# Optimization experiments

Hardware: AMD Instinct MI355X
Metric: run time of the kernel (lower is better)

## Reference

```python
import jax, jax.numpy as jnp
import numpy as np

# --- static forest structure: NT complete ternary trees of depth DEPTH ---
BR, DEPTH, NT = 3, 7, 64            # branching factor (=L), edge-levels, num trees
OFF = [(3 ** d - 1) // 2 for d in range(DEPTH + 2)]  # BFS level offsets within a tree
NPT = OFF[DEPTH + 1]                 # nodes per tree = 3280
DIM = NT * NPT                       # total nodes = 209920
C_DIM, NGEN, M_SYM = 8, 8, 128


def build_tree():
    """Returns pos, leaves, batch, roots, levels [(parent_idx, child_idx)], unique-parents per level."""
    base = (np.arange(NT) * NPT)[:, None]
    pos = np.zeros(DIM, dtype=np.int64)
    levels, upar = [], []
    for d in range(1, DEPTH + 1):
        loc = np.arange(OFF[d], OFF[d + 1])
        ch = (base + loc).ravel()                                 # children at depth d (tree-major)
        pa = (base + (OFF[d - 1] + (loc - OFF[d]) // BR)).ravel() # their parents
        pos[ch] = np.tile((loc - OFF[d]) % BR, NT)
        levels.append((pa, ch))
        upar.append((base + np.arange(OFF[d - 1], OFF[d])).ravel())  # unique parents of level d
    leaves = (base + np.arange(OFF[DEPTH], OFF[DEPTH + 1])).ravel()
    batch = np.repeat(np.arange(NT), NPT)
    roots = np.arange(NT) * NPT
    return pos, leaves, batch, roots, levels, upar


def setup_inputs() -> dict:
    key = jax.random.key(0)
    k1, k2, k3, k4, k5 = jax.random.split(key, 5)
    pos_np, leaves_np, batch_np, _, _, _ = build_tree()
    return {
        "lam_A": jax.random.uniform(k1, (C_DIM, C_DIM, BR, NGEN), dtype=jnp.float32),
        "lam_B": jax.random.uniform(k2, (C_DIM, M_SYM, NGEN), dtype=jnp.float32),
        "lam_Pi": jax.random.uniform(k3, (C_DIM, BR, NGEN), dtype=jnp.float32),
        "lam_SP": jax.random.uniform(k4, (BR, NGEN), dtype=jnp.float32),
        "x": jax.random.randint(k5, (DIM,), 0, M_SYM, dtype=jnp.int64),
        "pos": jnp.asarray(pos_np),
        "leaves": jnp.asarray(leaves_np),
        "batch": jnp.asarray(batch_np),
    }


def reference(lam_A, lam_B, lam_Pi, lam_SP, x, pos, leaves, batch):
    # ReversedUpwardDownward (mode='bu') of PosteriorHiddenTreeMarkovModel.
    A = jax.nn.softmax(lam_A, axis=0)   # (C,C,L,G): softmax over first state axis
    Bm = jax.nn.softmax(lam_B, axis=1)  # (C,M,G): softmax over symbols
    Pi = jax.nn.softmax(lam_Pi, axis=0) # (C,L,G)
    SP = jax.nn.softmax(lam_SP, axis=0) # (L,G)
    C, G = A.shape[0], A.shape[-1]
    _, _, _, roots, levels, upar = build_tree()  # static structure

    beta = jnp.zeros((DIM, C, G), lam_A.dtype)
    t_beta = jnp.zeros((DIM, C, G), lam_A.dtype)

    # --- leaves init ---
    Pi_leaves = Pi[:, pos[leaves]]            # (C,Nl,G)
    bl = jnp.transpose(Pi_leaves * Bm[:, x[leaves]], (1, 0, 2))  # (Nl,C,G)
    beta = beta.at[leaves].set(bl / bl.sum(1, keepdims=True))

    # --- upward pass (deepest level first) ---
    for (pa, ch), u in zip(reversed(levels), reversed(upar)):
        SP_ch = SP[pos[ch]][:, None, None, :]                 # (E,1,1,G)
        A_ch = jnp.transpose(A[:, :, pos[ch]], (2, 0, 1, 3))  # (E,C,C,G)
        tb = (SP_ch * A_ch * beta[ch][:, None]).sum(2)        # (E,C,G) sum over child state
        t_beta = t_beta.at[pa].add(tb)
        bu = t_beta[u] * jnp.transpose(Bm[:, x[u]], (1, 0, 2))
        beta = beta.at[u].set(bu / bu.sum(1, keepdims=True))

    # --- downward pass ---
    eps = jnp.zeros((DIM, C, G), lam_A.dtype)
    ell = jnp.zeros((DIM, G), lam_A.dtype)
    eps = eps.at[roots].set(beta[roots])
    for pa, ch in levels:
        SP_ch = SP[pos[ch]]                                   # (E,G)
        A_ch = jnp.transpose(A[:, :, pos[ch]], (2, 0, 1, 3))  # (E,C,C,G)
        trans = SP_ch[:, None, None, :] * A_ch
        ej = (eps[pa][:, :, None, :] * trans * beta[ch][:, None, :, :]
              / t_beta[pa][:, :, None, :])                    # (E,C,C,G) joint posterior
        eps = eps.at[ch].set(ej.sum(1))
        ell = ell.at[ch].add((ej * jnp.log(A_ch)).sum((1, 2))
                             + ej.sum((1, 2)) * jnp.log(SP_ch))
    ell = ell + (eps * jnp.transpose(Bm[:, x], (1, 0, 2))).sum(1)
    ell = ell.at[leaves].add((eps[leaves] * jnp.transpose(jnp.log(Pi_leaves), (1, 0, 2))).sum(1))
    return -jax.ops.segment_sum(ell, batch, num_segments=NT)  # (NT,G)
```

## Files before the change

### kernel.cpp

```cpp
#include <hip/hip_runtime.h>
#include <hip/hip_fp16.h>


namespace {

constexpr int kNPT = 3280;
constexpr int kRS  = 72;
constexpr int kAS  = 68;
constexpr unsigned kMAGIC  = 0x13579BDFu;
constexpr unsigned kMAGIC2 = 0x2468ACEFu;
__device__ __constant__ int LO[6] = {0, 1, 4, 13, 40, 121};
__device__ __constant__ int P3[5] = {1, 3, 9, 27, 81};

#define AGENT_LD(p)    __hip_atomic_load((p), __ATOMIC_RELAXED, __HIP_MEMORY_SCOPE_AGENT)
#define AGENT_ST(p, v) __hip_atomic_store((p), (v), __ATOMIC_RELAXED, __HIP_MEMORY_SCOPE_AGENT)

__device__ __forceinline__ void bm_row(const float* __restrict__ pBmg, int xv,
                                       float* m)
{
    const float4 r0 = *(const float4*)(pBmg + (xv << 3));
    const float4 r1 = *(const float4*)(pBmg + (xv << 3) + 4);
    m[0] = r0.x; m[1] = r0.y; m[2] = r0.z; m[3] = r0.w;
    m[4] = r1.x; m[5] = r1.y; m[6] = r1.z; m[7] = r1.w;
}

__device__ __forceinline__ void leaf_beta(const float* __restrict__ sPi,
                                          const float* __restrict__ pBmg,
                                          int p, int xv, int g, float* b)
{
    float m[8];
    bm_row(pBmg, xv, m);
    float s = 0.f;
    #pragma unroll
    for (int c = 0; c < 8; ++c) {
        b[c] = sPi[(c * 3 + p) * 8 + g] * m[c];
        s += b[c];
    }
    float ig = __builtin_amdgcn_rcpf(s);
    #pragma unroll
    for (int c = 0; c < 8; ++c) b[c] *= ig;
}

__device__ __forceinline__ float norm_mul(const float* __restrict__ pBmg,
                                          int xv, float* acc)
{
    float m[8];
    bm_row(pBmg, xv, m);
    float s = 0.f;
    #pragma unroll
    for (int i = 0; i < 8; ++i) { acc[i] *= m[i]; s += acc[i]; }
    return s;
}

__device__ __forceinline__ void matvec_acc(const float* __restrict__ arow,
                                           const float* __restrict__ bj,
                                           float spg, float* acc)
{
    #pragma unroll
    for (int j = 0; j < 8; ++j) {
        float4 a0 = *(const float4*)(arow + j * 8);
        float4 a1 = *(const float4*)(arow + j * 8 + 4);
        float cjv = spg * bj[j];
        acc[0] = fmaf(a0.x, cjv, acc[0]); acc[1] = fmaf(a0.y, cjv, acc[1]);
        acc[2] = fmaf(a0.z, cjv, acc[2]); acc[3] = fmaf(a0.w, cjv, acc[3]);
        acc[4] = fmaf(a1.x, cjv, acc[4]); acc[5] = fmaf(a1.y, cjv, acc[5]);
        acc[6] = fmaf(a1.z, cjv, acc[6]); acc[7] = fmaf(a1.w, cjv, acc[7]);
    }
}

__global__ __launch_bounds__(256, 2)
void fused(const float* __restrict__ lamA, const float* __restrict__ lamB,
           const float* __restrict__ lamPi, const float* __restrict__ lamSP,
           const int* __restrict__ x, float* __restrict__ out,
           unsigned* __restrict__ sy, float* __restrict__ bmG,
           float* __restrict__ b3, float* __restrict__ e3)
{
    const int tid = threadIdx.x, w = tid >> 6, lane = tid & 63;
    const int n = lane >> 3, g = lane & 7;
    __shared__ __align__(16) float sAg[24 * kAS];
    __shared__ __align__(16) float sLAg[24 * kAS];
    __shared__ float sPi[192], sLPi[192], sSP[24], sLSP[24];
    __shared__ float bW[4][40 * kRS];
    __shared__ __half bMidH[13 * 64];
    __shared__ float sMs[13 * 8];
    __shared__ unsigned char xW[4][124];
    unsigned* trCnt = sy + 32;
    unsigned* trFlg = sy + 2080;

    if (tid == 0) {
        if (blockIdx.x == 0) {
            for (int i = 0; i < 64; ++i) AGENT_ST(&trCnt[i * 32], 0u);
            __builtin_amdgcn_s_waitcnt(0);
            AGENT_ST(&sy[0], kMAGIC);
        }
        unsigned long sp = 0;
        while (AGENT_LD(&sy[0]) != kMAGIC) {
            if (++sp > (1UL << 24)) break;
            __builtin_amdgcn_s_sleep(2);
        }
    }
    __syncthreads();

    if (blockIdx.x == 0) {
        float* rr = &bW[0][0];
        int row = tid >> 2, part = tid & 3;
        int c = row >> 3, gg = row & 7, m0 = part * 32;
        float mx = -1e30f;
        for (int mm = 0; mm < 32; ++mm)
            mx = fmaxf(mx, lamB[(c * 128 + m0 + mm) * 8 + gg]);
        rr[tid] = mx;
        __syncthreads();
        float m4 = fmaxf(fmaxf(rr[row * 4], rr[row * 4 + 1]),
                         fmaxf(rr[row * 4 + 2], rr[row * 4 + 3]));
        float s = 0.f;
        for (int mm = 0; mm < 32; ++mm)
            s += expf(lamB[(c * 128 + m0 + mm) * 8 + gg] - m4);
        rr[256 + tid] = s;
        __syncthreads();
        float stot = rr[256 + row * 4] + rr[256 + row * 4 + 1]
                   + rr[256 + row * 4 + 2] + rr[256 + row * 4 + 3];
        float inv = 1.f / stot;
        for (int mm = 0; mm < 32; ++mm)
            AGENT_ST(&bmG[(gg * 128 + m0 + mm) * 8 + c],
                     expf(lamB[(c * 128 + m0 + mm) * 8 + gg] - m4) * inv);
        __syncthreads();
        if (tid == 0) AGENT_ST(&sy[4], kMAGIC2);
    }
    for (int col = tid; col < 192; col += 256) {
        int j = col / 24; int rem = col - j * 24; int p = rem >> 3; int gg = rem & 7;
        float v[8]; float mx = -1e30f;
        #pragma unroll
        for (int i = 0; i < 8; ++i) {
            v[i] = lamA[((i * 8 + j) * 3 + p) * 8 + gg];
            mx = fmaxf(mx, v[i]);
        }
        float s = 0.f;
        #pragma unroll
        for (int i = 0; i < 8; ++i) { v[i] = expf(v[i] - mx); s += v[i]; }
        float inv = 1.f / s;
        int base = (gg * 3 + p) * kAS + j * 8;
        #pragma unroll
        for (int i = 0; i < 8; ++i) {
            float sm = v[i] * inv;
            sAg[base + i]  = sm;
            sLAg[base + i] = sm * logf(sm);
        }
    }
    for (int col = tid; col < 24; col += 256) {
        int p = col >> 3; int gg = col & 7;
        float v[8]; float mx = -1e30f;
        #pragma unroll
        for (int c = 0; c < 8; ++c) {
            v[c] = lamPi[(c * 3 + p) * 8 + gg];
            mx = fmaxf(mx, v[c]);
        }
        float s = 0.f;
        #pragma unroll
        for (int c = 0; c < 8; ++c) { v[c] = expf(v[c] - mx); s += v[c]; }
        float inv = 1.f / s;
        #pragma unroll
        for (int c = 0; c < 8; ++c) {
            int idx = (c * 3 + p) * 8 + gg;
            float sm = v[c] * inv;
            sPi[idx]  = sm;
            sLPi[idx] = logf(sm);
        }
    }
    if (tid < 8) {
        int gg = tid;
        float v0 = lamSP[gg], v1 = lamSP[8 + gg], v2 = lamSP[16 + gg];
        float mx = fmaxf(v0, fmaxf(v1, v2));
        float e0 = expf(v0 - mx), e1 = expf(v1 - mx), e2 = expf(v2 - mx);
        float inv = 1.f / (e0 + e1 + e2);
        sSP[gg] = e0 * inv; sSP[8 + gg] = e1 * inv; sSP[16 + gg] = e2 * inv;
        sLSP[gg] = logf(e0 * inv); sLSP[8 + gg] = logf(e1 * inv); sLSP[16 + gg] = logf(e2 * inv);
    }
    if (tid == 0) {
        unsigned long sp = 0;
        while (AGENT_LD(&sy[4]) != kMAGIC2) {
            if (++sp > (1UL << 24)) break;
            __builtin_amdgcn_s_sleep(2);
        }
        __threadfence();
    }
    __syncthreads();

    const float* pBmg = bmG + (g << 10);
    const int t = blockIdx.x / 7, rb = blockIdx.x - t * 7;
    const int q = rb * 4 + w;
    const int id = t * 27 + q;
    const int xb = t * kNPT;
    float* bw = &bW[w][0];
    unsigned char* xw = &xW[w][0];

    if (q < 27) {
        for (int u = lane; u < 121; u += 64) {
            int gx;
            if (u == 0)       gx = 13 + q;
            else if (u < 4)   gx = 40  + q * 3  + (u - 1);
            else if (u < 13)  gx = 121 + q * 9  + (u - 4);
            else if (u < 40)  gx = 364 + q * 27 + (u - 13);
            else              gx = 1093 + q * 81 + (u - 40);
            xw[u] = (unsigned char)x[xb + gx];
        }
        __builtin_amdgcn_wave_barrier();

        for (int e = 3; e >= 0; --e) {
            int cnt = P3[e];
            for (int base = 0; base < cnt; base += 8) {
                int node = base + n;
                if (node < cnt) {
                    float acc[8];
                    #pragma unroll
                    for (int i = 0; i < 8; ++i) acc[i] = 0.f;
                    #pragma unroll
                    for (int k = 0; k < 3; ++k) {
                        float bj[8];
                        if (e == 3) {
                            leaf_beta(sPi, pBmg, k, xw[40 + 3 * node + k], g, bj);
                        } else {
                            int co = (LO[e + 1] + 3 * node + k) * kRS + g;
                            #pragma unroll
                            for (int j = 0; j < 8; ++j) bj[j] = bw[co + j * 8];
                        }
                        matvec_acc(&sAg[(g * 3 + k) * kAS], bj, sSP[k * 8 + g], acc);
                    }
                    if (e == 0) {
                        #pragma unroll
                        for (int i = 0; i < 8; ++i) bw[i * 8 + g] = acc[i];
                        float s = norm_mul(pBmg, xw[0], acc);
                        float ig = __builtin_amdgcn_rcpf(s);
                        #pragma unroll
                        for (int i = 0; i < 8; ++i)
                            AGENT_ST(&b3[id * 64 + g * 8 + i], acc[i] * ig);
                    } else {
                        int slot = LO[e] + node;
                        float s = norm_mul(pBmg, xw[slot], acc);
                        float ig = __builtin_amdgcn_rcpf(s);
                        int bo = slot * kRS + g;
                        #pragma unroll
                        for (int i = 0; i < 8; ++i) bw[bo + i * 8] = acc[i] * ig;
                        bw[slot * kRS + 64 + g] = s;
                    }
                }
            }
            __builtin_amdgcn_wave_barrier();
        }
        __builtin_amdgcn_s_waitcnt(0);
        if (lane == 0)
            __hip_atomic_fetch_add(&trCnt[t * 32], 1u, __ATOMIC_RELAXED,
                                   __HIP_MEMORY_SCOPE_AGENT);
    }

    if (rb == 6) {
        {
            unsigned long sp = 0;
            while (AGENT_LD(&trCnt[t * 32]) < 27u) {
                if (++sp > (1UL << 22)) break;
                __builtin_amdgcn_s_sleep(1);
            }
        }
        __threadfence();
        __syncthreads();

        float ellm = 0.f;
        const int vn = (w << 3) + n;

        for (int f = 2; f >= 0; --f) {
            int cnt = (f == 2) ? 9 : (f == 1 ? 3 : 1);
            int pl0 = (f == 2) ? 4 : (f == 1 ? 1 : 0);
            int cl0 = (f == 1) ? 4 : 1;
            int pi = vn;
            if (pi < cnt) {
                float acc[8];
                #pragma unroll
                for (int i = 0; i < 8; ++i) acc[i] = 0.f;
                #pragma unroll
                for (int k = 0; k < 3; ++k) {
                    float bj[8];
                    if (f == 2) {
                        const float* src = b3 + (t * 27 + 3 * pi + k) * 64 + g * 8;
                        float4 s0 = *(const float4*)(src);
                        float4 s1 = *(const float4*)(src + 4);
                        bj[0] = s0.x; bj[1] = s0.y; bj[2] = s0.z; bj[3] = s0.w;
                        bj[4] = s1.x; bj[5] = s1.y; bj[6] = s1.z; bj[7] = s1.w;
                    } else {
                        int co = (cl0 + 3 * pi + k) * 64 + g;
                        #pragma unroll
                        for (int j = 0; j < 8; ++j)
                            bj[j] = __half2float(bMidH[co + j * 8]);
                    }
                    matvec_acc(&sAg[(g * 3 + k) * kAS], bj, sSP[k * 8 + g], acc);
                }
                int slot = pl0 + pi;
                float s = norm_mul(pBmg, x[xb + slot], acc);
                float ig = __builtin_amdgcn_rcpf(s);
                int bo = slot * 64 + g;
                #pragma unroll
                for (int i = 0; i < 8; ++i)
                    bMidH[bo + i * 8] = __float2half(acc[i] * ig);
                sMs[slot * 8 + g] = s;
            }
            __syncthreads();
        }
        if (w == 0 && n == 0) {
            float m[8];
            bm_row(pBmg, x[xb], m);
            float invs = __builtin_amdgcn_rcpf(sMs[g]);
            #pragma unroll
            for (int c = 0; c < 8; ++c)
                ellm += __half2float(bMidH[c * 8 + g]) * m[c];
            #pragma unroll
            for (int c = 0; c < 8; ++c)
                bMidH[c * 8 + g] = __float2half(m[c] * invs);
        }
        __syncthreads();
        for (int f = 1; f <= 3; ++f) {
            int cnt = (f == 1) ? 3 : (f == 2 ? 9 : 27);
            int cl0 = (f == 1) ? 1 : (f == 2 ? 4 : 13);
            int pl0 = (f == 1) ? 0 : (f == 2 ? 1 : 4);
            int ci = vn;
            if (ci < cnt) {
                int p = ci % 3;
                int ps = (pl0 + ci / 3) * 64 + g;
                float r[8];
                #pragma unroll
                for (int i = 0; i < 8; ++i) r[i] = __half2float(bMidH[ps + i * 8]);
                float bj[8]; float sv = 0.f;
                if (f == 3) {
                    const float* src = b3 + (t * 27 + ci) * 64 + g * 8;
                    float4 s0 = *(const float4*)(src);
                    float4 s1 = *(const float4*)(src + 4);
                    bj[0] = s0.x; bj[1] = s0.y; bj[2] = s0.z; bj[3] = s0.w;
                    bj[4] = s1.x; bj[5] = s1.y; bj[6] = s1.z; bj[7] = s1.w;
                } else {
                    int co = (cl0 + ci) * 64 + g;
                    #pragma unroll
                    for (int j = 0; j < 8; ++j) bj[j] = __half2float(bMidH[co + j * 8]);
                    sv = sMs[(cl0 + ci) * 8 + g];
                }
                float spg = sSP[p * 8 + g];
                const float* arow = &sAg[(g * 3 + p) * kAS];
                const float* lrow = &sLAg[(g * 3 + p) * kAS];
                float esum = 0.f, lg = 0.f;
                float ev[8];
                #pragma unroll
                for (int j = 0; j < 8; ++j) {
                    float4 a0 = *(const float4*)(arow + j * 8);
                    float4 a1 = *(const float4*)(arow + j * 8 + 4);
                    float4 l0 = *(const float4*)(lrow + j * 8);
                    float4 l1 = *(const float4*)(lrow + j * 8 + 4);
                    float s1 = r[0] * a0.x; s1 = fmaf(r[1], a0.y, s1);
                    s1 = fmaf(r[2], a0.z, s1); s1 = fmaf(r[3], a0.w, s1);
                    s1 = fmaf(r[4], a1.x, s1); s1 = fmaf(r[5], a1.y, s1);
                    s1 = fmaf(r[6], a1.z, s1); s1 = fmaf(r[7], a1.w, s1);
                    float s2 = r[0] * l0.x; s2 = fmaf(r[1], l0.y, s2);
                    s2 = fmaf(r[2], l0.z, s2); s2 = fmaf(r[3], l0.w, s2);
                    s2 = fmaf(r[4], l1.x, s2); s2 = fmaf(r[5], l1.y, s2);
                    s2 = fmaf(r[6], l1.z, s2); s2 = fmaf(r[7], l1.w, s2);
                    float bs = spg * bj[j];
                    ev[j] = bs * s1;
                    lg    = fmaf(bs, s2, lg);
                    esum += ev[j];
                }
                lg = fmaf(esum, sLSP[p * 8 + g], lg);
                float Bmv[8];
                bm_row(pBmg, x[xb + cl0 + ci], Bmv);
                #pragma unroll
                for (int c = 0; c < 8; ++c)
                    lg = fmaf(ev[c], Bmv[c], lg);
                if (f == 3) {
                    #pragma unroll
                    for (int j = 0; j < 8; ++j)
                        AGENT_ST(&e3[(t * 27 + ci) * 64 + g * 8 + j], ev[j]);
                } else {
                    int co = (cl0 + ci) * 64 + g;
                    #pragma unroll
                    for (int j = 0; j < 8; ++j)
                        bMidH[co + j * 8] = __float2half(
                            ev[j] * Bmv[j] * __builtin_amdgcn_rcpf(bj[j] * sv));
                }
                ellm += lg;
            }
            __syncthreads();
        }
        ellm += __shfl_xor(ellm, 8);
        ellm += __shfl_xor(ellm, 16);
        ellm += __shfl_xor(ellm, 32);
        if (n == 0) atomicAdd(&out[t * 8 + g], -ellm);
        __builtin_amdgcn_s_waitcnt(0);
        __syncthreads();
        if (tid == 0) AGENT_ST(&trFlg[t * 32], kMAGIC2);
        if (q == 27) return;
    } else {
        unsigned long sp = 0;
        while (AGENT_LD(&trFlg[t * 32]) != kMAGIC2) {
            if (++sp > (1UL << 22)) break;
            __builtin_amdgcn_s_sleep(1);
        }
    }

    {
        int li = ((lane & 7) << 3) | (lane >> 3);
        bw[li] = AGENT_LD(&e3[id * 64 + lane]) * __builtin_amdgcn_rcpf(bw[li]);
    }
    __builtin_amdgcn_wave_barrier();

    float ell = 0.f;
    for (int e = 1; e <= 4; ++e) {
        int cnt = P3[e], pl0 = LO[e - 1];
        for (int base = 0; base < cnt; base += 8) {
            int ci = base + n;
            if (ci < cnt) {
                int p = ci % 3;
                int ps = (pl0 + ci / 3) * kRS + g;
                float r[8];
                #pragma unroll
                for (int i = 0; i < 8; ++i) r[i] = bw[ps + i * 8];
                float bj[8]; float sv = 0.f;
                int xv;
                if (e == 4) {
                    xv = xw[40 + ci];
                    leaf_beta(sPi, pBmg, p, xv, g, bj);
                } else {
                    int slot = LO[e] + ci;
                    xv = xw[slot];
                    int co = slot * kRS + g;
                    #pragma unroll
                    for (int j = 0; j < 8; ++j) bj[j] = bw[co + j * 8];
                    sv = bw[slot * kRS + 64 + g];
                }
                float spg = sSP[p * 8 + g];
                const float* arow = &sAg[(g * 3 + p) * kAS];
                const float* lrow = &sLAg[(g * 3 + p) * kAS];
                float esum = 0.f, lg = 0.f;
                float ev[8];
                #pragma unroll
                for (int j = 0; j < 8; ++j) {
                    float4 a0 = *(const float4*)(arow + j * 8);
                    float4 a1 = *(const float4*)(arow + j * 8 + 4);
                    float4 l0 = *(const float4*)(lrow + j * 8);
                    float4 l1 = *(const float4*)(lrow + j * 8 + 4);
                    float s1 = r[0] * a0.x; s1 = fmaf(r[1], a0.y, s1);
                    s1 = fmaf(r[2], a0.z, s1); s1 = fmaf(r[3], a0.w, s1);
                    s1 = fmaf(r[4], a1.x, s1); s1 = fmaf(r[5], a1.y, s1);
                    s1 = fmaf(r[6], a1.z, s1); s1 = fmaf(r[7], a1.w, s1);
                    float s2 = r[0] * l0.x; s2 = fmaf(r[1], l0.y, s2);
                    s2 = fmaf(r[2], l0.z, s2); s2 = fmaf(r[3], l0.w, s2);
                    s2 = fmaf(r[4], l1.x, s2); s2 = fmaf(r[5], l1.y, s2);
                    s2 = fmaf(r[6], l1.z, s2); s2 = fmaf(r[7], l1.w, s2);
                    float bs = spg * bj[j];
                    ev[j] = bs * s1;
                    lg    = fmaf(bs, s2, lg);
                    esum += ev[j];
                }
                lg = fmaf(esum, sLSP[p * 8 + g], lg);
                float Bmv[8];
                bm_row(pBmg, xv, Bmv);
                #pragma unroll
                for (int c = 0; c < 8; ++c)
                    lg = fmaf(ev[c], Bmv[c], lg);
                if (e < 4) {
                    int slot = LO[e] + ci;
                    int co = slot * kRS + g;
                    #pragma unroll
                    for (int j = 0; j < 8; ++j)
                        bw[co + j * 8] = ev[j] * Bmv[j]
                            * __builtin_amdgcn_rcpf(bj[j] * sv);
                } else {
                    #pragma unroll
                    for (int c = 0; c < 8; ++c)
                        lg = fmaf(ev[c], sLPi[(c * 3 + p) * 8 + g], lg);
                }
                ell += lg;
            }
        }
        __builtin_amdgcn_wave_barrier();
    }

    ell += __shfl_xor(ell, 8);
    ell += __shfl_xor(ell, 16);
    ell += __shfl_xor(ell, 32);
    if (n == 0) atomicAdd(&out[t * 8 + g], -ell);
}

}

extern "C" void kernel_launch(void* const* d_in, const int* in_sizes, int n_in,
                              void* d_out, int out_size, void* d_ws, size_t ws_size,
                              hipStream_t stream) {
    const float* lamA  = (const float*)d_in[0];
    const float* lamB  = (const float*)d_in[1];
    const float* lamPi = (const float*)d_in[2];
    const float* lamSP = (const float*)d_in[3];
    const int*   x     = (const int*)d_in[4];
    float* out = (float*)d_out;
    unsigned* sy  = (unsigned*)d_ws;
    float* bmG = (float*)d_ws + 8192;
    float* b3  = bmG + 8192;
    float* e3  = b3 + 1728 * 64;

    fused<<<dim3(448), dim3(256), 0, stream>>>(
        lamA, lamB, lamPi, lamSP, x, out, sy, bmG, b3, e3);
}
```

Measured before the change: 141.2 us.

## Split subtree work across two-wave blocks with a dedicated top-of-tree block

The kernel now launches four times as many blocks with half as many threads. Each block owns one subtree, with its two waves cooperating on 16 nodes at a time, so per-wave shared buffers become a single per-block buffer and wave barriers become block barriers. A separate block per tree handles the top levels and signals the subtree blocks through flags. The b3/e3 staging layout is transposed to match. The aim is more parallelism and latency hiding, at the cost of more cross-block spin-waiting and a dependence on enough blocks being resident at once.

New measurement: 195.7 us. 38.6% more time.

```diff
diff --git a/kernel.cpp b/kernel.cpp
--- a/kernel.cpp
+++ b/kernel.cpp
@@ -68,7 +68,7 @@
     }
 }
 
-__global__ __launch_bounds__(256, 2)
+__global__ __launch_bounds__(128, 2)
 void fused(const float* __restrict__ lamA, const float* __restrict__ lamB,
            const float* __restrict__ lamPi, const float* __restrict__ lamSP,
            const int* __restrict__ x, float* __restrict__ out,
@@ -77,13 +77,14 @@
 {
     const int tid = threadIdx.x, w = tid >> 6, lane = tid & 63;
     const int n = lane >> 3, g = lane & 7;
+    const int vn = (w << 3) + n;
     __shared__ __align__(16) float sAg[24 * kAS];
     __shared__ __align__(16) float sLAg[24 * kAS];
     __shared__ float sPi[192], sLPi[192], sSP[24], sLSP[24];
-    __shared__ float bW[4][40 * kRS];
+    __shared__ float bw[40 * kRS];
     __shared__ __half bMidH[13 * 64];
     __shared__ float sMs[13 * 8];
-    __shared__ unsigned char xW[4][124];
+    __shared__ unsigned char xw[124];
     unsigned* trCnt = sy + 32;
     unsigned* trFlg = sy + 2080;
 
@@ -102,31 +103,43 @@
     __syncthreads();
 
     if (blockIdx.x == 0) {
-        float* rr = &bW[0][0];
-        int row = tid >> 2, part = tid & 3;
-        int c = row >> 3, gg = row & 7, m0 = part * 32;
-        float mx = -1e30f;
-        for (int mm = 0; mm < 32; ++mm)
-            mx = fmaxf(mx, lamB[(c * 128 + m0 + mm) * 8 + gg]);
-        rr[tid] = mx;
-        __syncthreads();
-        float m4 = fmaxf(fmaxf(rr[row * 4], rr[row * 4 + 1]),
-                         fmaxf(rr[row * 4 + 2], rr[row * 4 + 3]));
-        float s = 0.f;
-        for (int mm = 0; mm < 32; ++mm)
-            s += expf(lamB[(c * 128 + m0 + mm) * 8 + gg] - m4);
-        rr[256 + tid] = s;
-        __syncthreads();
-        float stot = rr[256 + row * 4] + rr[256 + row * 4 + 1]
-                   + rr[256 + row * 4 + 2] + rr[256 + row * 4 + 3];
-        float inv = 1.f / stot;
-        for (int mm = 0; mm < 32; ++mm)
-            AGENT_ST(&bmG[(gg * 128 + m0 + mm) * 8 + c],
-                     expf(lamB[(c * 128 + m0 + mm) * 8 + gg] - m4) * inv);
+        float* rr = &bw[0];
+        for (int pp = tid; pp < 256; pp += 128) {
+            int row = pp >> 2, part = pp & 3;
+            int c = row >> 3, gg = row & 7, m0 = part * 32;
+            float mx = -1e30f;
+            for (int mm = 0; mm < 32; ++mm)
+                mx = fmaxf(mx, lamB[(c * 128 + m0 + mm) * 8 + gg]);
+            rr[pp] = mx;
+        }
+        __syncthreads();
+        for (int pp = tid; pp < 256; pp += 128) {
+            int row = pp >> 2, part = pp & 3;
+            int c = row >> 3, gg = row & 7, m0 = part * 32;
+            float m4 = fmaxf(fmaxf(rr[row * 4], rr[row * 4 + 1]),
+                             fmaxf(rr[row * 4 + 2], rr[row * 4 + 3]));
+            float s = 0.f;
+            for (int mm = 0; mm < 32; ++mm)
+                s += expf(lamB[(c * 128 + m0 + mm) * 8 + gg] - m4);
+            rr[256 + pp] = s;
+        }
+        __syncthreads();
+        for (int pp = tid; pp < 256; pp += 128) {
+            int row = pp >> 2, part = pp & 3;
+            int c = row >> 3, gg = row & 7, m0 = part * 32;
+            float m4 = fmaxf(fmaxf(rr[row * 4], rr[row * 4 + 1]),
+                             fmaxf(rr[row * 4 + 2], rr[row * 4 + 3]));
+            float stot = rr[256 + row * 4] + rr[256 + row * 4 + 1]
+                       + rr[256 + row * 4 + 2] + rr[256 + row * 4 + 3];
+            float inv = 1.f / stot;
+            for (int mm = 0; mm < 32; ++mm)
+                AGENT_ST(&bmG[(gg * 128 + m0 + mm) * 8 + c],
+                         expf(lamB[(c * 128 + m0 + mm) * 8 + gg] - m4) * inv);
+        }
         __syncthreads();
         if (tid == 0) AGENT_ST(&sy[4], kMAGIC2);
     }
-    for (int col = tid; col < 192; col += 256) {
+    for (int col = tid; col < 192; col += 128) {
         int j = col / 24; int rem = col - j * 24; int p = rem >> 3; int gg = rem & 7;
         float v[8]; float mx = -1e30f;
         #pragma unroll
@@ -146,7 +159,7 @@
             sLAg[base + i] = sm * logf(sm);
         }
     }
-    for (int col = tid; col < 24; col += 256) {
+    for (int col = tid; col < 24; col += 128) {
         int p = col >> 3; int gg = col & 7;
         float v[8]; float mx = -1e30f;
         #pragma unroll
@@ -186,29 +199,26 @@
     __syncthreads();
 
     const float* pBmg = bmG + (g << 10);
-    const int t = blockIdx.x / 7, rb = blockIdx.x - t * 7;
-    const int q = rb * 4 + w;
-    const int id = t * 27 + q;
+    const int t = blockIdx.x / 28, rb = blockIdx.x - t * 28;
+    const int id = t * 27 + rb;
     const int xb = t * kNPT;
-    float* bw = &bW[w][0];
-    unsigned char* xw = &xW[w][0];
-
-    if (q < 27) {
-        for (int u = lane; u < 121; u += 64) {
+
+    if (rb < 27) {
+        for (int u = tid; u < 121; u += 128) {
             int gx;
-            if (u == 0)       gx = 13 + q;
-            else if (u < 4)   gx = 40  + q * 3  + (u - 1);
-            else if (u < 13)  gx = 121 + q * 9  + (u - 4);
-            else if (u < 40)  gx = 364 + q * 27 + (u - 13);
-            else              gx = 1093 + q * 81 + (u - 40);
+            if (u == 0)       gx = 13 + rb;
+            else if (u < 4)   gx = 40  + rb * 3  + (u - 1);
+            else if (u < 13)  gx = 121 + rb * 9  + (u - 4);
+            else if (u < 40)  gx = 364 + rb * 27 + (u - 13);
+            else              gx = 1093 + rb * 81 + (u - 40);
             xw[u] = (unsigned char)x[xb + gx];
         }
-        __builtin_amdgcn_wave_barrier();
+        __syncthreads();
 
         for (int e = 3; e >= 0; --e) {
             int cnt = P3[e];
-            for (int base = 0; base < cnt; base += 8) {
-                int node = base + n;
+            for (int base = 0; base < cnt; base += 16) {
+                int node = base + vn;
                 if (node < cnt) {
                     float acc[8];
                     #pragma unroll
@@ -232,7 +242,7 @@
                         float ig = __builtin_amdgcn_rcpf(s);
                         #pragma unroll
                         for (int i = 0; i < 8; ++i)
-                            AGENT_ST(&b3[id * 64 + g * 8 + i], acc[i] * ig);
+                            AGENT_ST(&b3[id * 64 + i * 8 + g], acc[i] * ig);
                     } else {
                         int slot = LO[e] + node;
                         float s = norm_mul(pBmg, xw[slot], acc);
@@ -244,82 +254,175 @@
                     }
                 }
             }
-            __builtin_amdgcn_wave_barrier();
+            __syncthreads();
         }
         __builtin_amdgcn_s_waitcnt(0);
-        if (lane == 0)
+        if (tid == 0)
             __hip_atomic_fetch_add(&trCnt[t * 32], 1u, __ATOMIC_RELAXED,
                                    __HIP_MEMORY_SCOPE_AGENT);
-    }
-
-    if (rb == 6) {
+
         {
             unsigned long sp = 0;
-            while (AGENT_LD(&trCnt[t * 32]) < 27u) {
+            while (AGENT_LD(&trFlg[t * 32]) != kMAGIC2) {
                 if (++sp > (1UL << 22)) break;
                 __builtin_amdgcn_s_sleep(1);
             }
         }
-        __threadfence();
-        __syncthreads();
-
-        float ellm = 0.f;
-        const int vn = (w << 3) + n;
-
-        for (int f = 2; f >= 0; --f) {
-            int cnt = (f == 2) ? 9 : (f == 1 ? 3 : 1);
-            int pl0 = (f == 2) ? 4 : (f == 1 ? 1 : 0);
-            int cl0 = (f == 1) ? 4 : 1;
-            int pi = vn;
-            if (pi < cnt) {
-                float acc[8];
-                #pragma unroll
-                for (int i = 0; i < 8; ++i) acc[i] = 0.f;
-                #pragma unroll
-                for (int k = 0; k < 3; ++k) {
-                    float bj[8];
-                    if (f == 2) {
-                        const float* src = b3 + (t * 27 + 3 * pi + k) * 64 + g * 8;
-                        float4 s0 = *(const float4*)(src);
-                        float4 s1 = *(const float4*)(src + 4);
-                        bj[0] = s0.x; bj[1] = s0.y; bj[2] = s0.z; bj[3] = s0.w;
-                        bj[4] = s1.x; bj[5] = s1.y; bj[6] = s1.z; bj[7] = s1.w;
+        if (w == 0)
+            bw[lane] = AGENT_LD(&e3[id * 64 + lane]) * __builtin_amdgcn_rcpf(bw[lane]);
+        __syncthreads();
+
+        float ell = 0.f;
+        for (int e = 1; e <= 4; ++e) {
+            int cnt = P3[e], pl0 = LO[e - 1];
+            for (int base = 0; base < cnt; base += 16) {
+                int ci = base + vn;
+                if (ci < cnt) {
+                    int p = ci % 3;
+                    int ps = (pl0 + ci / 3) * kRS + g;
+                    float r[8];
+                    #pragma unroll
+                    for (int i = 0; i < 8; ++i) r[i] = bw[ps + i * 8];
+                    float bj[8]; float sv = 0.f;
+                    float Bmv[8];
+                    if (e == 4) {
+                        int xv = xw[40 + ci];
+                        bm_row(pBmg, xv, Bmv);
+                        float s = 0.f;
+                        #pragma unroll
+                        for (int c = 0; c < 8; ++c) {
+                            bj[c] = sPi[(c * 3 + p) * 8 + g] * Bmv[c];
+                            s += bj[c];
+                        }
+                        float ig = __builtin_amdgcn_rcpf(s);
+                        #pragma unroll
+                        for (int c = 0; c < 8; ++c) bj[c] *= ig;
                     } else {
-                        int co = (cl0 + 3 * pi + k) * 64 + g;
+                        int slot = LO[e] + ci;
+                        bm_row(pBmg, xw[slot], Bmv);
+                        int co = slot * kRS + g;
+                        #pragma unroll
+                        for (int j = 0; j < 8; ++j) bj[j] = bw[co + j * 8];
+                        sv = bw[slot * kRS + 64 + g];
+                    }
+                    float spg = sSP[p * 8 + g];
+                    const float* arow = &sAg[(g * 3 + p) * kAS];
+                    const float* lrow = &sLAg[(g * 3 + p) * kAS];
+                    float esum = 0.f, lg = 0.f;
+                    float ev[8];
+                    #pragma unroll
+                    for (int j = 0; j < 8; ++j) {
+                        float4 a0 = *(const float4*)(arow + j * 8);
+                        float4 a1 = *(const float4*)(arow + j * 8 + 4);
+                        float4 l0 = *(const float4*)(lrow + j * 8);
+                        float4 l1 = *(const float4*)(lrow + j * 8 + 4);
+                        float s1 = r[0] * a0.x; s1 = fmaf(r[1], a0.y, s1);
+                        s1 = fmaf(r[2], a0.z, s1); s1 = fmaf(r[3], a0.w, s1);
+                        s1 = fmaf(r[4], a1.x, s1); s1 = fmaf(r[5], a1.y, s1);
+                        s1 = fmaf(r[6], a1.z, s1); s1 = fmaf(r[7], a1.w, s1);
+                        float s2 = r[0] * l0.x; s2 = fmaf(r[1], l0.y, s2);
+                        s2 = fmaf(r[2], l0.z, s2); s2 = fmaf(r[3], l0.w, s2);
+                        s2 = fmaf(r[4], l1.x, s2); s2 = fmaf(r[5], l1.y, s2);
+                        s2 = fmaf(r[6], l1.z, s2); s2 = fmaf(r[7], l1.w, s2);
+                        float bs = spg * bj[j];
+                        ev[j] = bs * s1;
+                        lg    = fmaf(bs, s2, lg);
+                        esum += ev[j];
+                    }
+                    lg = fmaf(esum, sLSP[p * 8 + g], lg);
+                    #pragma unroll
+                    for (int c = 0; c < 8; ++c)
+                        lg = fmaf(ev[c], Bmv[c], lg);
+                    if (e < 4) {
+                        int slot = LO[e] + ci;
+                        int co = slot * kRS + g;
                         #pragma unroll
                         for (int j = 0; j < 8; ++j)
-                            bj[j] = __half2float(bMidH[co + j * 8]);
+                            bw[co + j * 8] = ev[j] * Bmv[j]
+                                * __builtin_amdgcn_rcpf(bj[j] * sv);
+                    } else {
+                        #pragma unroll
+                        for (int c = 0; c < 8; ++c)
+                            lg = fmaf(ev[c], sLPi[(c * 3 + p) * 8 + g], lg);
                     }
-                    matvec_acc(&sAg[(g * 3 + k) * kAS], bj, sSP[k * 8 + g], acc);
+                    ell += lg;
                 }
-                int slot = pl0 + pi;
-                float s = norm_mul(pBmg, x[xb + slot], acc);
-                float ig = __builtin_amdgcn_rcpf(s);
-                int bo = slot * 64 + g;
-                #pragma unroll
-                for (int i = 0; i < 8; ++i)
-                    bMidH[bo + i * 8] = __float2half(acc[i] * ig);
-                sMs[slot * 8 + g] = s;
             }
             __syncthreads();
         }
-        if (w == 0 && n == 0) {
-            float m[8];
-            bm_row(pBmg, x[xb], m);
-            float invs = __builtin_amdgcn_rcpf(sMs[g]);
+
+        ell += __shfl_xor(ell, 8);
+        ell += __shfl_xor(ell, 16);
+        ell += __shfl_xor(ell, 32);
+        if (n == 0) atomicAdd(&out[t * 8 + g], -ell);
+        return;
+    }
+
+    {
+        unsigned long sp = 0;
+        while (AGENT_LD(&trCnt[t * 32]) < 27u) {
+            if (++sp > (1UL << 22)) break;
+            __builtin_amdgcn_s_sleep(1);
+        }
+    }
+    __threadfence();
+    __syncthreads();
+
+    float ellm = 0.f;
+
+    for (int f = 2; f >= 0; --f) {
+        int cnt = (f == 2) ? 9 : (f == 1 ? 3 : 1);
+        int pl0 = (f == 2) ? 4 : (f == 1 ? 1 : 0);
+        int cl0 = (f == 1) ? 4 : 1;
+        int pi = vn;
+        if (pi < cnt) {
+            float acc[8];
             #pragma unroll
-            for (int c = 0; c < 8; ++c)
-                ellm += __half2float(bMidH[c * 8 + g]) * m[c];
+            for (int i = 0; i < 8; ++i) acc[i] = 0.f;
             #pragma unroll
-            for (int c = 0; c < 8; ++c)
-                bMidH[c * 8 + g] = __float2half(m[c] * invs);
-        }
-        __syncthreads();
-        for (int f = 1; f <= 3; ++f) {
-            int cnt = (f == 1) ? 3 : (f == 2 ? 9 : 27);
-            int cl0 = (f == 1) ? 1 : (f == 2 ? 4 : 13);
-            int pl0 = (f == 1) ? 0 : (f == 2 ? 1 : 4);
-            int ci = vn;
+            for (int k = 0; k < 3; ++k) {
+                float bj[8];
+                if (f == 2) {
+                    const float* src = b3 + (t * 27 + 3 * pi + k) * 64 + g;
+                    #pragma unroll
+                    for (int j = 0; j < 8; ++j) bj[j] = src[j * 8];
+                } else {
+                    int co = (cl0 + 3 * pi + k) * 64 + g;
+                    #pragma unroll
+                    for (int j = 0; j < 8; ++j)
+                        bj[j] = __half2float(bMidH[co + j * 8]);
+                }
+                matvec_acc(&sAg[(g * 3 + k) * kAS], bj, sSP[k * 8 + g], acc);
+            }
+            int slot = pl0 + pi;
+            float s = norm_mul(pBmg, x[xb + slot], acc);
+            float ig = __builtin_amdgcn_rcpf(s);
+            int bo = slot * 64 + g;
+            #pragma unroll
+            for (int i = 0; i < 8; ++i)
+                bMidH[bo + i * 8] = __float2half(acc[i] * ig);
+            sMs[slot * 8 + g] = s;
+        }
+        __syncthreads();
+    }
+    if (w == 0 && n == 0) {
+        float m[8];
+        bm_row(pBmg, x[xb], m);
+        float invs = __builtin_amdgcn_rcpf(sMs[g]);
+        #pragma unroll
+        for (int c = 0; c < 8; ++c)
+            ellm += __half2float(bMidH[c * 8 + g]) * m[c];
+        #pragma unroll
+        for (int c = 0; c < 8; ++c)
+            bMidH[c * 8 + g] = __float2half(m[c] * invs);
+    }
+    __syncthreads();
+    for (int f = 1; f <= 3; ++f) {
+        int cnt = (f == 1) ? 3 : (f == 2 ? 9 : 27);
+        int cl0 = (f == 1) ? 1 : (f == 2 ? 4 : 13);
+        int pl0 = (f == 1) ? 0 : (f == 2 ? 1 : 4);
+        for (int base = 0; base < cnt; base += 16) {
+            int ci = base + vn;
             if (ci < cnt) {
                 int p = ci % 3;
                 int ps = (pl0 + ci / 3) * 64 + g;
@@ -328,11 +431,9 @@
                 for (int i = 0; i < 8; ++i) r[i] = __half2float(bMidH[ps + i * 8]);
                 float bj[8]; float sv = 0.f;
                 if (f == 3) {
-                    const float* src = b3 + (t * 27 + ci) * 64 + g * 8;
-                    float4 s0 = *(const float4*)(src);
-                    float4 s1 = *(const float4*)(src + 4);
-                    bj[0] = s0.x; bj[1] = s0.y; bj[2] = s0.z; bj[3] = s0.w;
-                    bj[4] = s1.x; bj[5] = s1.y; bj[6] = s1.z; bj[7] = s1.w;
+                    const float* src = b3 + (t * 27 + ci) * 64 + g;
+                    #pragma unroll
+                    for (int j = 0; j < 8; ++j) bj[j] = src[j * 8];
                 } else {
                     int co = (cl0 + ci) * 64 + g;
                     #pragma unroll
@@ -372,7 +473,7 @@
                 if (f == 3) {
                     #pragma unroll
                     for (int j = 0; j < 8; ++j)
-                        AGENT_ST(&e3[(t * 27 + ci) * 64 + g * 8 + j], ev[j]);
+                        AGENT_ST(&e3[(t * 27 + ci) * 64 + j * 8 + g], ev[j]);
                 } else {
                     int co = (cl0 + ci) * 64 + g;
                     #pragma unroll
@@ -382,106 +483,16 @@
                 }
                 ellm += lg;
             }
-            __syncthreads();
-        }
-        ellm += __shfl_xor(ellm, 8);
-        ellm += __shfl_xor(ellm, 16);
-        ellm += __shfl_xor(ellm, 32);
-        if (n == 0) atomicAdd(&out[t * 8 + g], -ellm);
-        __builtin_amdgcn_s_waitcnt(0);
-        __syncthreads();
-        if (tid == 0) AGENT_ST(&trFlg[t * 32], kMAGIC2);
-        if (q == 27) return;
-    } else {
-        unsigned long sp = 0;
-        while (AGENT_LD(&trFlg[t * 32]) != kMAGIC2) {
-            if (++sp > (1UL << 22)) break;
-            __builtin_amdgcn_s_sleep(1);
-        }
-    }
-
-    {
-        int li = ((lane & 7) << 3) | (lane >> 3);
-        bw[li] = AGENT_LD(&e3[id * 64 + lane]) * __builtin_amdgcn_rcpf(bw[li]);
-    }
-    __builtin_amdgcn_wave_barrier();
-
-    float ell = 0.f;
-    for (int e = 1; e <= 4; ++e) {
-        int cnt = P3[e], pl0 = LO[e - 1];
-        for (int base = 0; base < cnt; base += 8) {
-            int ci = base + n;
-            if (ci < cnt) {
-                int p = ci % 3;
-                int ps = (pl0 + ci / 3) * kRS + g;
-                float r[8];
-                #pragma unroll
-                for (int i = 0; i < 8; ++i) r[i] = bw[ps + i * 8];
-                float bj[8]; float sv = 0.f;
-                int xv;
-                if (e == 4) {
-                    xv = xw[40 + ci];
-                    leaf_beta(sPi, pBmg, p, xv, g, bj);
-                } else {
-                    int slot = LO[e] + ci;
-                    xv = xw[slot];
-                    int co = slot * kRS + g;
-                    #pragma unroll
-                    for (int j = 0; j < 8; ++j) bj[j] = bw[co + j * 8];
-                    sv = bw[slot * kRS + 64 + g];
-                }
-                float spg = sSP[p * 8 + g];
-                const float* arow = &sAg[(g * 3 + p) * kAS];
-                const float* lrow = &sLAg[(g * 3 + p) * kAS];
-                float esum = 0.f, lg = 0.f;
-                float ev[8];
-                #pragma unroll
-                for (int j = 0; j < 8; ++j) {
-                    float4 a0 = *(const float4*)(arow + j * 8);
-                    float4 a1 = *(const float4*)(arow + j * 8 + 4);
-                    float4 l0 = *(const float4*)(lrow + j * 8);
-                    float4 l1 = *(const float4*)(lrow + j * 8 + 4);
-                    float s1 = r[0] * a0.x; s1 = fmaf(r[1], a0.y, s1);
-                    s1 = fmaf(r[2], a0.z, s1); s1 = fmaf(r[3], a0.w, s1);
-                    s1 = fmaf(r[4], a1.x, s1); s1 = fmaf(r[5], a1.y, s1);
-                    s1 = fmaf(r[6], a1.z, s1); s1 = fmaf(r[7], a1.w, s1);
-                    float s2 = r[0] * l0.x; s2 = fmaf(r[1], l0.y, s2);
-                    s2 = fmaf(r[2], l0.z, s2); s2 = fmaf(r[3], l0.w, s2);
-                    s2 = fmaf(r[4], l1.x, s2); s2 = fmaf(r[5], l1.y, s2);
-                    s2 = fmaf(r[6], l1.z, s2); s2 = fmaf(r[7], l1.w, s2);
-                    float bs = spg * bj[j];
-                    ev[j] = bs * s1;
-                    lg    = fmaf(bs, s2, lg);
-                    esum += ev[j];
-                }
-                lg = fmaf(esum, sLSP[p * 8 + g], lg);
-                float Bmv[8];
-                bm_row(pBmg, xv, Bmv);
-                #pragma unroll
-                for (int c = 0; c < 8; ++c)
-                    lg = fmaf(ev[c], Bmv[c], lg);
-                if (e < 4) {
-                    int slot = LO[e] + ci;
-                    int co = slot * kRS + g;
-                    #pragma unroll
-                    for (int j = 0; j < 8; ++j)
-                        bw[co + j * 8] = ev[j] * Bmv[j]
-                            * __builtin_amdgcn_rcpf(bj[j] * sv);
-                } else {
-                    #pragma unroll
-                    for (int c = 0; c < 8; ++c)
-                        lg = fmaf(ev[c], sLPi[(c * 3 + p) * 8 + g], lg);
-                }
-                ell += lg;
-            }
-        }
-        __builtin_amdgcn_wave_barrier();
-    }
-
-    ell += __shfl_xor(ell, 8);
-    ell += __shfl_xor(ell, 16);
-    ell += __shfl_xor(ell, 32);
-    if (n == 0) atomicAdd(&out[t * 8 + g], -ell);
+        }
+        __syncthreads();
+    }
+    ellm += __shfl_xor(ellm, 8);
+    ellm += __shfl_xor(ellm, 16);
+    ellm += __shfl_xor(ellm, 32);
+    if (n == 0) atomicAdd(&out[t * 8 + g], -ellm);
+    __builtin_amdgcn_s_waitcnt(0);
+    __syncthreads();
+    if (tid == 0) AGENT_ST(&trFlg[t * 32], kMAGIC2);
 }
 
 }
@@ -500,6 +511,6 @@
     float* b3  = bmG + 8192;
     float* e3  = b3 + 1728 * 64;
 
-    fused<<<dim3(448), dim3(256), 0, stream>>>(
+    fused<<<dim3(1792), dim3(128), 0, stream>>>(
         lamA, lamB, lamPi, lamSP, x, out, sy, bmG, b3, e3);
 }
```

## Transpose LDS beta/Pi layouts to state-contiguous and read A from global for upward matvec

Applied to the files above, without the earlier changes.

Reorganises the per-wave beta scratch and the Pi/logPi tables so each lane's eight states are contiguous, which allows 128-bit LDS reads and writes, and pads the row stride to 76. Block 0 also writes the softmaxed transition matrix to a global buffer. The upward matvec then reads A through the cache instead of LDS, and the b3/e3 exchange layouts are transposed to match. The intent is fewer LDS instructions and bank conflicts. The cost is global loads in the hot upward loop and a wider publish barrier that now waits on block 0's A writes.

After: 197.7 us. 40.1% more time.

```diff
diff --git a/kernel.cpp b/kernel.cpp
--- a/kernel.cpp
+++ b/kernel.cpp
@@ -5,7 +5,7 @@
 namespace {
 
 constexpr int kNPT = 3280;
-constexpr int kRS  = 72;
+constexpr int kRS  = 76;
 constexpr int kAS  = 68;
 constexpr unsigned kMAGIC  = 0x13579BDFu;
 constexpr unsigned kMAGIC2 = 0x2468ACEFu;
@@ -15,6 +15,20 @@
 #define AGENT_LD(p)    __hip_atomic_load((p), __ATOMIC_RELAXED, __HIP_MEMORY_SCOPE_AGENT)
 #define AGENT_ST(p, v) __hip_atomic_store((p), (v), __ATOMIC_RELAXED, __HIP_MEMORY_SCOPE_AGENT)
 
+__device__ __forceinline__ void rd8(const float* __restrict__ p, float* d)
+{
+    float4 a = *(const float4*)p;
+    float4 b = *(const float4*)(p + 4);
+    d[0] = a.x; d[1] = a.y; d[2] = a.z; d[3] = a.w;
+    d[4] = b.x; d[5] = b.y; d[6] = b.z; d[7] = b.w;
+}
+
+__device__ __forceinline__ void wr8(float* __restrict__ p, const float* s)
+{
+    *(float4*)p       = make_float4(s[0], s[1], s[2], s[3]);
+    *(float4*)(p + 4) = make_float4(s[4], s[5], s[6], s[7]);
+}
+
 __device__ __forceinline__ void bm_row(const float* __restrict__ pBmg, int xv,
                                        float* m)
 {
@@ -24,18 +38,16 @@
     m[4] = r1.x; m[5] = r1.y; m[6] = r1.z; m[7] = r1.w;
 }
 
-__device__ __forceinline__ void leaf_beta(const float* __restrict__ sPi,
+__device__ __forceinline__ void leaf_beta(const float* __restrict__ piRow,
                                           const float* __restrict__ pBmg,
-                                          int p, int xv, int g, float* b)
-{
-    float m[8];
+                                          int xv, float* b)
+{
+    float m[8], pi[8];
     bm_row(pBmg, xv, m);
+    rd8(piRow, pi);
     float s = 0.f;
     #pragma unroll
-    for (int c = 0; c < 8; ++c) {
-        b[c] = sPi[(c * 3 + p) * 8 + g] * m[c];
-        s += b[c];
-    }
+    for (int c = 0; c < 8; ++c) { b[c] = pi[c] * m[c]; s += b[c]; }
     float ig = __builtin_amdgcn_rcpf(s);
     #pragma unroll
     for (int c = 0; c < 8; ++c) b[c] *= ig;
@@ -68,19 +80,47 @@
     }
 }
 
+__device__ __forceinline__ void dn_body(const float* r, const float* bj, float spg,
+                                        const float* __restrict__ arow,
+                                        const float* __restrict__ lrow,
+                                        float* ev, float& esum, float& lg)
+{
+    #pragma unroll
+    for (int j = 0; j < 8; ++j) {
+        float4 a0 = *(const float4*)(arow + j * 8);
+        float4 a1 = *(const float4*)(arow + j * 8 + 4);
+        float4 l0 = *(const float4*)(lrow + j * 8);
+        float4 l1 = *(const float4*)(lrow + j * 8 + 4);
+        float s1 = r[0] * a0.x; s1 = fmaf(r[1], a0.y, s1);
+        s1 = fmaf(r[2], a0.z, s1); s1 = fmaf(r[3], a0.w, s1);
+        s1 = fmaf(r[4], a1.x, s1); s1 = fmaf(r[5], a1.y, s1);
+        s1 = fmaf(r[6], a1.z, s1); s1 = fmaf(r[7], a1.w, s1);
+        float s2 = r[0] * l0.x; s2 = fmaf(r[1], l0.y, s2);
+        s2 = fmaf(r[2], l0.z, s2); s2 = fmaf(r[3], l0.w, s2);
+        s2 = fmaf(r[4], l1.x, s2); s2 = fmaf(r[5], l1.y, s2);
+        s2 = fmaf(r[6], l1.z, s2); s2 = fmaf(r[7], l1.w, s2);
+        float bs = spg * bj[j];
+        ev[j] = bs * s1;
+        lg    = fmaf(bs, s2, lg);
+        esum += ev[j];
+    }
+}
+
 __global__ __launch_bounds__(256, 2)
 void fused(const float* __restrict__ lamA, const float* __restrict__ lamB,
            const float* __restrict__ lamPi, const float* __restrict__ lamSP,
            const int* __restrict__ x, float* __restrict__ out,
            unsigned* __restrict__ sy, float* __restrict__ bmG,
-           float* __restrict__ b3, float* __restrict__ e3)
+           float* __restrict__ b3, float* __restrict__ e3,
+           float* __restrict__ aG)
 {
     const int tid = threadIdx.x, w = tid >> 6, lane = tid & 63;
     const int n = lane >> 3, g = lane & 7;
     __shared__ __align__(16) float sAg[24 * kAS];
     __shared__ __align__(16) float sLAg[24 * kAS];
-    __shared__ float sPi[192], sLPi[192], sSP[24], sLSP[24];
-    __shared__ float bW[4][40 * kRS];
+    __shared__ __align__(16) float sPi[192], sLPi[192];
+    __shared__ float sSP[24], sLSP[24];
+    __shared__ __align__(16) float bW[4][40 * kRS];
     __shared__ __half bMidH[13 * 64];
     __shared__ float sMs[13 * 8];
     __shared__ unsigned char xW[4][124];
@@ -124,7 +164,6 @@
             AGENT_ST(&bmG[(gg * 128 + m0 + mm) * 8 + c],
                      expf(lamB[(c * 128 + m0 + mm) * 8 + gg] - m4) * inv);
         __syncthreads();
-        if (tid == 0) AGENT_ST(&sy[4], kMAGIC2);
     }
     for (int col = tid; col < 192; col += 256) {
         int j = col / 24; int rem = col - j * 24; int p = rem >> 3; int gg = rem & 7;
@@ -139,11 +178,13 @@
         for (int i = 0; i < 8; ++i) { v[i] = expf(v[i] - mx); s += v[i]; }
         float inv = 1.f / s;
         int base = (gg * 3 + p) * kAS + j * 8;
+        int gbase = (gg * 3 + p) * 64 + j * 8;
         #pragma unroll
         for (int i = 0; i < 8; ++i) {
             float sm = v[i] * inv;
             sAg[base + i]  = sm;
             sLAg[base + i] = sm * logf(sm);
+            if (blockIdx.x == 0) AGENT_ST(&aG[gbase + i], sm);
         }
     }
     for (int col = tid; col < 24; col += 256) {
@@ -160,7 +201,7 @@
         float inv = 1.f / s;
         #pragma unroll
         for (int c = 0; c < 8; ++c) {
-            int idx = (c * 3 + p) * 8 + gg;
+            int idx = (gg * 3 + p) * 8 + c;
             float sm = v[c] * inv;
             sPi[idx]  = sm;
             sLPi[idx] = logf(sm);
@@ -174,6 +215,13 @@
         float inv = 1.f / (e0 + e1 + e2);
         sSP[gg] = e0 * inv; sSP[8 + gg] = e1 * inv; sSP[16 + gg] = e2 * inv;
         sLSP[gg] = logf(e0 * inv); sLSP[8 + gg] = logf(e1 * inv); sLSP[16 + gg] = logf(e2 * inv);
+    }
+    if (blockIdx.x == 0) {
+        __syncthreads();
+        if (tid == 0) {
+            __builtin_amdgcn_s_waitcnt(0);
+            AGENT_ST(&sy[4], kMAGIC2);
+        }
     }
     if (tid == 0) {
         unsigned long sp = 0;
@@ -217,29 +265,29 @@
                     for (int k = 0; k < 3; ++k) {
                         float bj[8];
                         if (e == 3) {
-                            leaf_beta(sPi, pBmg, k, xw[40 + 3 * node + k], g, bj);
+                            leaf_beta(sPi + (g * 3 + k) * 8, pBmg,
+                                      xw[40 + 3 * node + k], bj);
                         } else {
-                            int co = (LO[e + 1] + 3 * node + k) * kRS + g;
-                            #pragma unroll
-                            for (int j = 0; j < 8; ++j) bj[j] = bw[co + j * 8];
+                            rd8(bw + (LO[e + 1] + 3 * node + k) * kRS + g * 8, bj);
                         }
-                        matvec_acc(&sAg[(g * 3 + k) * kAS], bj, sSP[k * 8 + g], acc);
+                        matvec_acc(aG + (g * 3 + k) * 64, bj, sSP[k * 8 + g], acc);
                     }
                     if (e == 0) {
                         #pragma unroll
-                        for (int i = 0; i < 8; ++i) bw[i * 8 + g] = acc[i];
+                        for (int i = 0; i < 8; ++i) bw[g * 8 + i] = acc[i];
                         float s = norm_mul(pBmg, xw[0], acc);
                         float ig = __builtin_amdgcn_rcpf(s);
                         #pragma unroll
                         for (int i = 0; i < 8; ++i)
-                            AGENT_ST(&b3[id * 64 + g * 8 + i], acc[i] * ig);
+                            AGENT_ST(&b3[id * 64 + i * 8 + g], acc[i] * ig);
                     } else {
                         int slot = LO[e] + node;
                         float s = norm_mul(pBmg, xw[slot], acc);
                         float ig = __builtin_amdgcn_rcpf(s);
-                        int bo = slot * kRS + g;
+                        float be[8];
                         #pragma unroll
-                        for (int i = 0; i < 8; ++i) bw[bo + i * 8] = acc[i] * ig;
+                        for (int i = 0; i < 8; ++i) be[i] = acc[i] * ig;
+                        wr8(bw + slot * kRS + g * 8, be);
                         bw[slot * kRS + 64 + g] = s;
                     }
                 }
@@ -279,18 +327,16 @@
                 for (int k = 0; k < 3; ++k) {
                     float bj[8];
                     if (f == 2) {
-                        const float* src = b3 + (t * 27 + 3 * pi + k) * 64 + g * 8;
-                        float4 s0 = *(const float4*)(src);
-                        float4 s1 = *(const float4*)(src + 4);
-                        bj[0] = s0.x; bj[1] = s0.y; bj[2] = s0.z; bj[3] = s0.w;
-                        bj[4] = s1.x; bj[5] = s1.y; bj[6] = s1.z; bj[7] = s1.w;
+                        const float* src = b3 + (t * 27 + 3 * pi + k) * 64 + g;
+                        #pragma unroll
+                        for (int j = 0; j < 8; ++j) bj[j] = src[j * 8];
                     } else {
                         int co = (cl0 + 3 * pi + k) * 64 + g;
                         #pragma unroll
                         for (int j = 0; j < 8; ++j)
                             bj[j] = __half2float(bMidH[co + j * 8]);
                     }
-                    matvec_acc(&sAg[(g * 3 + k) * kAS], bj, sSP[k * 8 + g], acc);
+                    matvec_acc(aG + (g * 3 + k) * 64, bj, sSP[k * 8 + g], acc);
                 }
                 int slot = pl0 + pi;
                 float s = norm_mul(pBmg, x[xb + slot], acc);
@@ -328,51 +374,29 @@
                 for (int i = 0; i < 8; ++i) r[i] = __half2float(bMidH[ps + i * 8]);
                 float bj[8]; float sv = 0.f;
                 if (f == 3) {
-                    const float* src = b3 + (t * 27 + ci) * 64 + g * 8;
-                    float4 s0 = *(const float4*)(src);
-                    float4 s1 = *(const float4*)(src + 4);
-                    bj[0] = s0.x; bj[1] = s0.y; bj[2] = s0.z; bj[3] = s0.w;
-                    bj[4] = s1.x; bj[5] = s1.y; bj[6] = s1.z; bj[7] = s1.w;
+                    const float* src = b3 + (t * 27 + ci) * 64 + g;
+                    #pragma unroll
+                    for (int j = 0; j < 8; ++j) bj[j] = src[j * 8];
                 } else {
                     int co = (cl0 + ci) * 64 + g;
                     #pragma unroll
                     for (int j = 0; j < 8; ++j) bj[j] = __half2float(bMidH[co + j * 8]);
                     sv = sMs[(cl0 + ci) * 8 + g];
                 }
-                float spg = sSP[p * 8 + g];
-                const float* arow = &sAg[(g * 3 + p) * kAS];
-                const float* lrow = &sLAg[(g * 3 + p) * kAS];
-                float esum = 0.f, lg = 0.f;
-                float ev[8];
-                #pragma unroll
-                for (int j = 0; j < 8; ++j) {
-                    float4 a0 = *(const float4*)(arow + j * 8);
-                    float4 a1 = *(const float4*)(arow + j * 8 + 4);
-                    float4 l0 = *(const float4*)(lrow + j * 8);
-                    float4 l1 = *(const float4*)(lrow + j * 8 + 4);
-                    float s1 = r[0] * a0.x; s1 = fmaf(r[1], a0.y, s1);
-                    s1 = fmaf(r[2], a0.z, s1); s1 = fmaf(r[3], a0.w, s1);
-                    s1 = fmaf(r[4], a1.x, s1); s1 = fmaf(r[5], a1.y, s1);
-                    s1 = fmaf(r[6], a1.z, s1); s1 = fmaf(r[7], a1.w, s1);
-                    float s2 = r[0] * l0.x; s2 = fmaf(r[1], l0.y, s2);
-                    s2 = fmaf(r[2], l0.z, s2); s2 = fmaf(r[3], l0.w, s2);
-                    s2 = fmaf(r[4], l1.x, s2); s2 = fmaf(r[5], l1.y, s2);
-                    s2 = fmaf(r[6], l1.z, s2); s2 = fmaf(r[7], l1.w, s2);
-                    float bs = spg * bj[j];
-                    ev[j] = bs * s1;
-                    lg    = fmaf(bs, s2, lg);
-                    esum += ev[j];
-                }
-                lg = fmaf(esum, sLSP[p * 8 + g], lg);
                 float Bmv[8];
                 bm_row(pBmg, x[xb + cl0 + ci], Bmv);
+                float ev[8]; float esum = 0.f, lg = 0.f;
+                dn_body(r, bj, sSP[p * 8 + g],
+                        &sAg[(g * 3 + p) * kAS], &sLAg[(g * 3 + p) * kAS],
+                        ev, esum, lg);
+                lg = fmaf(esum, sLSP[p * 8 + g], lg);
                 #pragma unroll
                 for (int c = 0; c < 8; ++c)
                     lg = fmaf(ev[c], Bmv[c], lg);
                 if (f == 3) {
                     #pragma unroll
                     for (int j = 0; j < 8; ++j)
-                        AGENT_ST(&e3[(t * 27 + ci) * 64 + g * 8 + j], ev[j]);
+                        AGENT_ST(&e3[(t * 27 + ci) * 64 + j * 8 + g], ev[j]);
                 } else {
                     int co = (cl0 + ci) * 64 + g;
                     #pragma unroll
@@ -413,64 +437,45 @@
             int ci = base + n;
             if (ci < cnt) {
                 int p = ci % 3;
-                int ps = (pl0 + ci / 3) * kRS + g;
                 float r[8];
-                #pragma unroll
-                for (int i = 0; i < 8; ++i) r[i] = bw[ps + i * 8];
-                float bj[8]; float sv = 0.f;
-                int xv;
+                rd8(bw + (pl0 + ci / 3) * kRS + g * 8, r);
+                float bj[8], Bmv[8]; float sv = 0.f;
                 if (e == 4) {
-                    xv = xw[40 + ci];
-                    leaf_beta(sPi, pBmg, p, xv, g, bj);
+                    bm_row(pBmg, xw[40 + ci], Bmv);
+                    float pi[8];
+                    rd8(sPi + (g * 3 + p) * 8, pi);
+                    float s = 0.f;
+                    #pragma unroll
+                    for (int c = 0; c < 8; ++c) { bj[c] = pi[c] * Bmv[c]; s += bj[c]; }
+                    float ig = __builtin_amdgcn_rcpf(s);
+                    #pragma unroll
+                    for (int c = 0; c < 8; ++c) bj[c] *= ig;
                 } else {
                     int slot = LO[e] + ci;
-                    xv = xw[slot];
-                    int co = slot * kRS + g;
-                    #pragma unroll
-                    for (int j = 0; j < 8; ++j) bj[j] = bw[co + j * 8];
+                    bm_row(pBmg, xw[slot], Bmv);
+                    rd8(bw + slot * kRS + g * 8, bj);
                     sv = bw[slot * kRS + 64 + g];
                 }
-                float spg = sSP[p * 8 + g];
-                const float* arow = &sAg[(g * 3 + p) * kAS];
-                const float* lrow = &sLAg[(g * 3 + p) * kAS];
-                float esum = 0.f, lg = 0.f;
-                float ev[8];
+                float ev[8]; float esum = 0.f, lg = 0.f;
+                dn_body(r, bj, sSP[p * 8 + g],
+                        &sAg[(g * 3 + p) * kAS], &sLAg[(g * 3 + p) * kAS],
+                        ev, esum, lg);
+                lg = fmaf(esum, sLSP[p * 8 + g], lg);
                 #pragma unroll
-                for (int j = 0; j < 8; ++j) {
-                    float4 a0 = *(const float4*)(arow + j * 8);
-                    float4 a1 = *(const float4*)(arow + j * 8 + 4);
-                    float4 l0 = *(const float4*)(lrow + j * 8);
-                    float4 l1 = *(const float4*)(lrow + j * 8 + 4);
-                    float s1 = r[0] * a0.x; s1 = fmaf(r[1], a0.y, s1);
-                    s1 = fmaf(r[2], a0.z, s1); s1 = fmaf(r[3], a0.w, s1);
-                    s1 = fmaf(r[4], a1.x, s1); s1 = fmaf(r[5], a1.y, s1);
-                    s1 = fmaf(r[6], a1.z, s1); s1 = fmaf(r[7], a1.w, s1);
-                    float s2 = r[0] * l0.x; s2 = fmaf(r[1], l0.y, s2);
-                    s2 = fmaf(r[2], l0.z, s2); s2 = fmaf(r[3], l0.w, s2);
-                    s2 = fmaf(r[4], l1.x, s2); s2 = fmaf(r[5], l1.y, s2);
-                    s2 = fmaf(r[6], l1.z, s2); s2 = fmaf(r[7], l1.w, s2);
-                    float bs = spg * bj[j];
-                    ev[j] = bs * s1;
-                    lg    = fmaf(bs, s2, lg);
-                    esum += ev[j];
-                }
-                lg = fmaf(esum, sLSP[p * 8 + g], lg);
-                float Bmv[8];
-                bm_row(pBmg, xv, Bmv);
-                #pragma unroll
-                for (int c = 0; c < 8; ++c)
-                    lg = fmaf(ev[c], Bmv[c], lg);
+                for (int c = 0; c < 8; ++c) lg = fmaf(ev[c], Bmv[c], lg);
                 if (e < 4) {
                     int slot = LO[e] + ci;
-                    int co = slot * kRS + g;
+                    float nb[8];
                     #pragma unroll
                     for (int j = 0; j < 8; ++j)
-                        bw[co + j * 8] = ev[j] * Bmv[j]
-                            * __builtin_amdgcn_rcpf(bj[j] * sv);
+                        nb[j] = ev[j] * Bmv[j] * __builtin_amdgcn_rcpf(bj[j] * sv);
+                    wr8(bw + slot * kRS + g * 8, nb);
                 } else {
+                    float lpi[8];
+                    rd8(sLPi + (g * 3 + p) * 8, lpi);
                     #pragma unroll
                     for (int c = 0; c < 8; ++c)
-                        lg = fmaf(ev[c], sLPi[(c * 3 + p) * 8 + g], lg);
+                        lg = fmaf(ev[c], lpi[c], lg);
                 }
                 ell += lg;
             }
@@ -499,7 +504,8 @@
     float* bmG = (float*)d_ws + 8192;
     float* b3  = bmG + 8192;
     float* e3  = b3 + 1728 * 64;
+    float* aG  = e3 + 1728 * 64;
 
     fused<<<dim3(448), dim3(256), 0, stream>>>(
-        lamA, lamB, lamPi, lamSP, x, out, sy, bmG, b3, e3);
-}
+        lamA, lamB, lamPi, lamSP, x, out, sy, bmG, b3, e3, aG);
+}
```
